# Kernel optimization log

Measured on AMD Instinct MI355X. Metric: run time of the kernel, lower is better.

The kernel has to match this reference:

```python
import jax, jax.numpy as jnp
import numpy as np

H, SK, SV, PK, PV = 12, 16, 16, 4, 8
SCALAR_DIM, PAIR_DIM = 384, 128
SIZES = [SK*H, SK*H, SV*H, PK*H*3, PK*H*3, PV*H*3]  # qkv split sizes
N_LOGITS = 3
SS = (N_LOGITS * SK) ** -0.5                 # scalar logit scale
PS = (N_LOGITS * PK * 4.5) ** -0.5           # point logit scale
PBS = N_LOGITS ** -0.5                       # pair bias scale
EPS = 1e-8


def setup_inputs() -> dict:
    key = jax.random.key(0)
    ks = jax.random.split(key, 16)
    b, n = 1, 768
    scalar_feats = jax.random.normal(ks[0], (b, n, SCALAR_DIM), jnp.float32)
    pair_feats = jax.random.normal(ks[1], (b, n, n, PAIR_DIM), jnp.float32)
    rotations = jax.random.normal(ks[2], (b, n, 3, 3), jnp.float32)
    translations = jax.random.normal(ks[3], (b, n, 3), jnp.float32)
    mask = jnp.ones((b, n), dtype=bool)
    d_qkv = sum(SIZES)
    sc = SCALAR_DIM ** -0.5
    Wqkv = jax.random.normal(ks[4], (SCALAR_DIM, d_qkv), jnp.float32) * sc
    Wpb = jax.random.normal(ks[5], (PAIR_DIM, H), jnp.float32) * PAIR_DIM ** -0.5
    point_weights = jnp.full((1, H, 1, 1), float(np.log(np.e - 1.0)), jnp.float32)
    dim_out = H * (PAIR_DIM + SV + 4 * PV)  # 2112
    Wout = jax.random.normal(ks[6], (dim_out, SCALAR_DIM), jnp.float32) * dim_out ** -0.5
    bout = jnp.zeros((SCALAR_DIM,), jnp.float32)
    Wp1 = jax.random.normal(ks[7], (3 * H, PAIR_DIM), jnp.float32) * (3 * H) ** -0.5
    bp1 = jnp.zeros((PAIR_DIM,), jnp.float32)
    Wp2 = jax.random.normal(ks[8], (PAIR_DIM, PAIR_DIM), jnp.float32) * PAIR_DIM ** -0.5
    bp2 = jnp.zeros((PAIR_DIM,), jnp.float32)
    return dict(scalar_feats=scalar_feats, pair_feats=pair_feats, rotations=rotations,
                translations=translations, mask=mask, Wqkv=Wqkv, Wpb=Wpb,
                point_weights=point_weights, Wout=Wout, bout=bout,
                Wp1=Wp1, bp1=bp1, Wp2=Wp2, bp2=bp2)


def _heads(x, b, n, d):
    # b n (h d) -> b h n d
    return x.reshape(b, n, H, d).transpose(0, 2, 1, 3)


def _merge(x):
    # b h n d -> b n (h d)
    b, h, n, d = x.shape
    return x.transpose(0, 2, 1, 3).reshape(b, n, h * d)


def ipa_forward(scalar_feats, pair_feats, rotations, translations, mask,
                Wqkv, Wpb, point_weights, Wout, bout, Wp1, bp1, Wp2, bp2):
    b, n, _ = scalar_feats.shape
    qkv = scalar_feats @ Wqkv
    offs = np.cumsum([0] + SIZES)
    qs, ks_, vs, qp, kp, vp = [qkv[..., offs[i]:offs[i + 1]] for i in range(6)]
    qs, ks_, vs = _heads(qs, b, n, SK), _heads(ks_, b, n, SK), _heads(vs, b, n, SV)

    def to_global_points(p, d):
        p = p.reshape(b, n, H * d, 3)                       # ... (d c) -> ... d c
        p = jnp.einsum('bixy,bidy->bidx', rotations, p) + translations[:, :, None, :]
        return p.reshape(b, n, H, d, 3).transpose(0, 2, 1, 3, 4)  # b h n d 3

    qp, kp = to_global_points(qp, PK), to_global_points(kp, PK)
    vp = to_global_points(vp, PV)

    scalar_logits = jnp.einsum('bhid,bhjd->bhij', qs, ks_)
    pair_bias = jnp.einsum('bijd,dh->bhij', pair_feats, Wpb)
    point_logits = jnp.einsum('bhidc,bhjdc->bhij', qp, kp) * jax.nn.softplus(point_weights)

    m2 = mask[:, None, :, None] & mask[:, None, None, :]    # b 1 i j
    neg = -jnp.finfo(scalar_logits.dtype).max
    scalar_logits = jnp.where(m2, scalar_logits, neg)
    point_logits = jnp.where(m2, point_logits, neg)
    pair_bias = jnp.where(m2, pair_bias, neg)

    attn = jax.nn.softmax(SS * scalar_logits + PS * point_logits + PBS * pair_bias, axis=-1)

    res_scalar = jnp.einsum('bhij,bhjd->bhid', attn, vs)
    res_pair = jnp.einsum('bhij,bijd->bhid', attn, pair_feats)
    res_pts = jnp.einsum('bhij,bhjdc->bhidc', attn, vp)
    # inverse rigid: R^T (p - t)
    local = jnp.einsum('biyx,bhidy->bhidx', rotations,
                       res_pts - translations[:, None, :, None, :])
    pts_norm = jnp.sqrt(jnp.sum(local ** 2, axis=-1) + EPS)  # safe_norm

    feats = jnp.concatenate([
        _merge(res_scalar),                                   # b n h*SV
        _merge(res_pair),                                     # b n h*PAIR_DIM
        _merge(local.reshape(b, H, n, PV * 3)),               # b n h*PV*3
        _merge(pts_norm),                                     # b n h*PV
    ], axis=-1)
    scalar_out = feats @ Wout + bout

    edge = jnp.concatenate([attn,
                            jax.nn.softmax(point_logits, axis=-1),
                            jax.nn.softmax(scalar_logits, axis=-1)], axis=1)
    edge = edge.transpose(0, 2, 3, 1)                         # b i j (3h)
    pair_out = jax.nn.gelu(edge @ Wp1 + bp1, approximate=False) @ Wp2 + bp2
    return scalar_out, pair_out


def reference(scalar_feats, pair_feats, rotations, translations, mask,
              Wqkv, Wpb, point_weights, Wout, bout, Wp1, bp1, Wp2, bp2):
    return ipa_forward(scalar_feats, pair_feats, rotations, translations, mask,
                       Wqkv, Wpb, point_weights, Wout, bout, Wp1, bp1, Wp2, bp2)
```

## Files before the change

### kernel.cpp

```cpp
#include <hip/hip_runtime.h>
#include <hip/hip_bf16.h>
#include <math.h>

#define NRES 768
#define NH 12
#define DQKV 1152
#define PAIRD 128
#define SCD 384
#define DOUTF 2112

#define SS_C 0.14433756729740643f
#define PS_C 0.13608276348795434f
#define PBS_C 0.5773502691896258f

typedef __attribute__((ext_vector_type(4))) float f32x4;
typedef __attribute__((ext_vector_type(8))) short s16x8;

__device__ __forceinline__ unsigned short f2bf(float x) {
  union { float f; unsigned u; } v; v.f = x;
  unsigned r = (v.u + 0x7fffu + ((v.u >> 16) & 1u)) >> 16;
  return (unsigned short)r;
}

__global__ __launch_bounds__(256) void gemm_f32(
    const float* __restrict__ A, const float* __restrict__ B,
    const float* __restrict__ bias, float* __restrict__ C,
    int M, int Nn, int K)
{
  __shared__ __align__(16) float As[16][68];
  __shared__ __align__(16) float Bs[16][68];
  int t = threadIdx.x;
  int m0 = blockIdx.y * 64, n0 = blockIdx.x * 64;
  int tx = t & 15, ty = t >> 4;
  float acc[4][4] = {};
  int am = t >> 2, ak = (t & 3) * 4;
  int bk = t >> 4, bn = (t & 15) * 4;
  for (int k0 = 0; k0 < K; k0 += 16) {
    float4 a4 = *(const float4*)(A + (size_t)(m0 + am) * K + k0 + ak);
    As[ak + 0][am] = a4.x; As[ak + 1][am] = a4.y;
    As[ak + 2][am] = a4.z; As[ak + 3][am] = a4.w;
    float4 b4 = *(const float4*)(B + (size_t)(k0 + bk) * Nn + n0 + bn);
    *(float4*)&Bs[bk][bn] = b4;
    __syncthreads();
#pragma unroll
    for (int k = 0; k < 16; ++k) {
      float4 av = *(float4*)&As[k][ty * 4];
      float4 bv = *(float4*)&Bs[k][tx * 4];
      float ar[4] = {av.x, av.y, av.z, av.w};
      float br[4] = {bv.x, bv.y, bv.z, bv.w};
#pragma unroll
      for (int r = 0; r < 4; ++r)
#pragma unroll
        for (int c = 0; c < 4; ++c)
          acc[r][c] += ar[r] * br[c];
    }
    __syncthreads();
  }
#pragma unroll
  for (int r = 0; r < 4; ++r) {
    int m = m0 + ty * 4 + r;
#pragma unroll
    for (int c = 0; c < 4; ++c) {
      int n = n0 + tx * 4 + c;
      float v = acc[r][c];
      if (bias) v += bias[n];
      C[(size_t)m * Nn + n] = v;
    }
  }
}

__global__ __launch_bounds__(256) void wt_kernel(
    const float* __restrict__ W, unsigned short* __restrict__ Wt)
{
  __shared__ float tile[32][33];
  int k0 = blockIdx.x * 32, n0 = blockIdx.y * 32;
  int t = threadIdx.x;
  int x = t & 31, y = t >> 5;
#pragma unroll
  for (int r = 0; r < 32; r += 8)
    tile[y + r][x] = W[(size_t)(k0 + y + r) * SCD + n0 + x];
  __syncthreads();
#pragma unroll
  for (int r = 0; r < 32; r += 8)
    Wt[(size_t)(n0 + y + r) * DOUTF + k0 + x] = f2bf(tile[x][y + r]);
}

__global__ __launch_bounds__(192) void points_kernel(
    const float* __restrict__ qkv, const float* __restrict__ rot,
    const float* __restrict__ trans, float* __restrict__ QP,
    float* __restrict__ KP, float* __restrict__ VP)
{
  int i = blockIdx.x;
  int t = threadIdx.x;
  const float* R = rot + (size_t)i * 9;
  const float* T = trans + (size_t)i * 3;
  int base; float* outp;
  if (t < 48) { int h = t >> 2, d = t & 3; base = 576 + (h * 4 + d) * 3;
    outp = QP + ((size_t)h * NRES + i) * 12 + d * 3; }
  else if (t < 96) { int u = t - 48; int h = u >> 2, d = u & 3; base = 720 + (h * 4 + d) * 3;
    outp = KP + ((size_t)h * NRES + i) * 12 + d * 3; }
  else { int u = t - 96; int h = u >> 3, d = u & 7; base = 864 + (h * 8 + d) * 3;
    outp = VP + ((size_t)h * NRES + i) * 24 + d * 3; }
  const float* p = qkv + (size_t)i * DQKV + base;
  float p0 = p[0], p1 = p[1], p2 = p[2];
#pragma unroll
  for (int x = 0; x < 3; ++x)
    outp[x] = R[x * 3 + 0] * p0 + R[x * 3 + 1] * p1 + R[x * 3 + 2] * p2 + T[x];
}

__global__ __launch_bounds__(256) void vt_kernel(
    const float* __restrict__ qkv, const float* __restrict__ VP,
    unsigned short* __restrict__ Vt)
{
  int b = blockIdx.x;
  int h = b / 48, o = b % 48;
  int t = threadIdx.x;
  for (int p = 0; p < 3; ++p) {
    int j = p * 256 + t;
    float v;
    if (o < 16) v = qkv[(size_t)j * DQKV + 384 + h * 16 + o];
    else if (o < 40) v = VP[((size_t)h * NRES + j) * 24 + (o - 16)];
    else v = 0.f;
    Vt[((size_t)h * 48 + o) * NRES + j] = f2bf(v);
  }
}

__global__ __launch_bounds__(256) void pair_bias_kernel(
    const float* __restrict__ pair, const float* __restrict__ Wpb,
    float* __restrict__ Lb)
{
  __shared__ __align__(16) unsigned short Bt[64][136];
  int jt = blockIdx.x, i = blockIdx.y;
  int j0 = jt * 64;
  int t = threadIdx.x;
  int lane = t & 63, w = t >> 6;
  int n15 = lane & 15, q = lane >> 4;
  s16x8 wf[4];
#pragma unroll
  for (int ks = 0; ks < 4; ++ks) {
#pragma unroll
    for (int jj = 0; jj < 8; ++jj) {
      int k = ks * 32 + q * 8 + jj;
      float v = (n15 < 12) ? Wpb[k * 12 + n15] : 0.f;
      wf[ks][jj] = (short)f2bf(v);
    }
  }
  {
    int dq = t & 31, jb = t >> 5;
    for (int p = 0; p < 8; ++p) {
      int j = p * 8 + jb;
      float4 v = *(const float4*)(pair + ((size_t)i * NRES + j0 + j) * PAIRD + dq * 4);
      unsigned lo = (unsigned)f2bf(v.x) | ((unsigned)f2bf(v.y) << 16);
      unsigned hi = (unsigned)f2bf(v.z) | ((unsigned)f2bf(v.w) << 16);
      uint2 pk; pk.x = lo; pk.y = hi;
      *(uint2*)&Bt[j][dq * 4] = pk;
    }
  }
  __syncthreads();
  f32x4 acc = {0.f, 0.f, 0.f, 0.f};
  int m = w * 16 + n15;
#pragma unroll
  for (int ks = 0; ks < 4; ++ks) {
    s16x8 af = *(const s16x8*)&Bt[m][ks * 32 + q * 8];
    acc = __builtin_amdgcn_mfma_f32_16x16x32_bf16(af, wf[ks], acc, 0, 0, 0);
  }
  if (n15 < 12) {
    int j = j0 + w * 16 + q * 4;
    float4 st; st.x = acc[0]; st.y = acc[1]; st.z = acc[2]; st.w = acc[3];
    *(float4*)(Lb + ((size_t)n15 * NRES + i) * NRES + j) = st;
  }
}

__global__ __launch_bounds__(256) void logits_softmax_kernel(
    const float* __restrict__ qkv, const float* __restrict__ QP,
    const float* __restrict__ KP, const float* __restrict__ pw,
    const float* __restrict__ Lb, unsigned short* __restrict__ attn_b,
    unsigned short* __restrict__ sp_b, unsigned short* __restrict__ ss_b)
{
  int i = blockIdx.x, h = blockIdx.y;
  int t = threadIdx.x;
  __shared__ float q_sh[28];
  if (t < 28) {
    if (t < 16) q_sh[t] = qkv[(size_t)i * DQKV + h * 16 + t];
    else q_sh[t] = QP[((size_t)h * NRES + i) * 12 + (t - 16)];
  }
  __syncthreads();
  float spw = log1pf(expf(pw[h]));
  size_t off = ((size_t)h * NRES + i) * NRES;
  float s[3], p[3], c[3];
#pragma unroll
  for (int e = 0; e < 3; ++e) {
    int j = t + e * 256;
    float kr[16];
    const float* kq = qkv + (size_t)j * DQKV + 192 + h * 16;
    *(float4*)&kr[0]  = *(const float4*)(kq + 0);
    *(float4*)&kr[4]  = *(const float4*)(kq + 4);
    *(float4*)&kr[8]  = *(const float4*)(kq + 8);
    *(float4*)&kr[12] = *(const float4*)(kq + 12);
    float sv = 0.f;
#pragma unroll
    for (int d = 0; d < 16; ++d) sv += q_sh[d] * kr[d];
    float kp[12];
    const float* kpp = KP + ((size_t)h * NRES + j) * 12;
    *(float4*)&kp[0] = *(const float4*)(kpp + 0);
    *(float4*)&kp[4] = *(const float4*)(kpp + 4);
    *(float4*)&kp[8] = *(const float4*)(kpp + 8);
    float pv = 0.f;
#pragma unroll
    for (int d = 0; d < 12; ++d) pv += q_sh[16 + d] * kp[d];
    pv *= spw;
    float bv = Lb[off + j];
    s[e] = sv; p[e] = pv;
    c[e] = SS_C * sv + PS_C * pv + PBS_C * bv;
  }
  __shared__ float redmax[4][3];
  __shared__ float redsum[4][3];
  float ms = fmaxf(fmaxf(s[0], s[1]), s[2]);
  float mp = fmaxf(fmaxf(p[0], p[1]), p[2]);
  float mc = fmaxf(fmaxf(c[0], c[1]), c[2]);
#pragma unroll
  for (int o = 32; o > 0; o >>= 1) {
    ms = fmaxf(ms, __shfl_down(ms, o));
    mp = fmaxf(mp, __shfl_down(mp, o));
    mc = fmaxf(mc, __shfl_down(mc, o));
  }
  int wv = t >> 6;
  if ((t & 63) == 0) { redmax[wv][0] = ms; redmax[wv][1] = mp; redmax[wv][2] = mc; }
  __syncthreads();
  ms = fmaxf(fmaxf(redmax[0][0], redmax[1][0]), fmaxf(redmax[2][0], redmax[3][0]));
  mp = fmaxf(fmaxf(redmax[0][1], redmax[1][1]), fmaxf(redmax[2][1], redmax[3][1]));
  mc = fmaxf(fmaxf(redmax[0][2], redmax[1][2]), fmaxf(redmax[2][2], redmax[3][2]));
  float es[3], ep[3], ec[3];
  float sums = 0.f, sump = 0.f, sumc = 0.f;
#pragma unroll
  for (int e = 0; e < 3; ++e) {
    es[e] = expf(s[e] - ms); sums += es[e];
    ep[e] = expf(p[e] - mp); sump += ep[e];
    ec[e] = expf(c[e] - mc); sumc += ec[e];
  }
#pragma unroll
  for (int o = 32; o > 0; o >>= 1) {
    sums += __shfl_down(sums, o);
    sump += __shfl_down(sump, o);
    sumc += __shfl_down(sumc, o);
  }
  if ((t & 63) == 0) { redsum[wv][0] = sums; redsum[wv][1] = sump; redsum[wv][2] = sumc; }
  __syncthreads();
  sums = redsum[0][0] + redsum[1][0] + redsum[2][0] + redsum[3][0];
  sump = redsum[0][1] + redsum[1][1] + redsum[2][1] + redsum[3][1];
  sumc = redsum[0][2] + redsum[1][2] + redsum[2][2] + redsum[3][2];
  float rs = 1.f / sums, rp = 1.f / sump, rc = 1.f / sumc;
#pragma unroll
  for (int e = 0; e < 3; ++e) {
    int j = t + e * 256;
    ss_b[off + j]   = f2bf(es[e] * rs);
    sp_b[off + j]   = f2bf(ep[e] * rp);
    attn_b[off + j] = f2bf(ec[e] * rc);
  }
}

__global__ __launch_bounds__(192) void res_sv_kernel(
    const unsigned short* __restrict__ attn, const unsigned short* __restrict__ Vt,
    float* __restrict__ res_sv)
{
  __shared__ __align__(16) unsigned short A_lds[16][72];
  __shared__ __align__(16) unsigned short B_lds[48][72];
  int it = blockIdx.x, h = blockIdx.y;
  int i0 = it * 16;
  int t = threadIdx.x;
  int lane = t & 63, w = t >> 6;
  int n15 = lane & 15, q = lane >> 4;
  f32x4 acc = {0.f, 0.f, 0.f, 0.f};
  for (int jt = 0; jt < 12; ++jt) {
    int j0 = jt * 64;
    __syncthreads();
    for (int idx = t; idx < 512; idx += 192) {
      int r = idx >> 5, j2 = idx & 31;
      *(unsigned*)&A_lds[r][j2 * 2] =
          *(const unsigned*)&attn[((size_t)h * NRES + i0 + r) * NRES + j0 + j2 * 2];
    }
    for (int idx = t; idx < 1536; idx += 192) {
      int o = idx >> 5, j2 = idx & 31;
      *(unsigned*)&B_lds[o][j2 * 2] =
          *(const unsigned*)&Vt[((size_t)h * 48 + o) * NRES + j0 + j2 * 2];
    }
    __syncthreads();
#pragma unroll
    for (int ks = 0; ks < 2; ++ks) {
      s16x8 af = *(const s16x8*)&A_lds[n15][ks * 32 + q * 8];
      s16x8 bf = *(const s16x8*)&B_lds[w * 16 + n15][ks * 32 + q * 8];
      acc = __builtin_amdgcn_mfma_f32_16x16x32_bf16(af, bf, acc, 0, 0, 0);
    }
  }
  int o = w * 16 + n15;
  if (o < 40) {
#pragma unroll
    for (int r = 0; r < 4; ++r) {
      int i = i0 + q * 4 + r;
      res_sv[((size_t)h * NRES + i) * 40 + o] = acc[r];
    }
  }
}

__global__ __launch_bounds__(256) void res_pair_kernel(
    const unsigned short* __restrict__ attn, const float* __restrict__ pair,
    float* __restrict__ res_pair)
{
  __shared__ __align__(16) unsigned short A_lds[16][72];
  __shared__ __align__(16) unsigned short B_lds[64][132];
  int i = blockIdx.x;
  int t = threadIdx.x;
  int lane = t & 63, w = t >> 6;
  int n15 = lane & 15, q = lane >> 4;
  for (int idx = t; idx < 4 * 72; idx += 256)
    A_lds[12 + idx / 72][idx % 72] = 0;
  f32x4 acc[2];
  acc[0] = (f32x4){0.f, 0.f, 0.f, 0.f};
  acc[1] = (f32x4){0.f, 0.f, 0.f, 0.f};
  for (int jt = 0; jt < 12; ++jt) {
    int j0 = jt * 64;
    __syncthreads();
    for (int idx = t; idx < 384; idx += 256) {
      int r = idx >> 5, j2 = idx & 31;
      *(unsigned*)&A_lds[r][j2 * 2] =
          *(const unsigned*)&attn[((size_t)r * NRES + i) * NRES + j0 + j2 * 2];
    }
    {
      int oq = t & 31, jb = t >> 5;
      for (int p = 0; p < 8; ++p) {
        int j = p * 8 + jb;
        float4 v = *(const float4*)(pair + ((size_t)i * NRES + j0 + j) * PAIRD + oq * 4);
        unsigned lo = (unsigned)f2bf(v.x) | ((unsigned)f2bf(v.y) << 16);
        unsigned hi = (unsigned)f2bf(v.z) | ((unsigned)f2bf(v.w) << 16);
        uint2 pk; pk.x = lo; pk.y = hi;
        *(uint2*)&B_lds[j][oq * 4] = pk;
      }
    }
    __syncthreads();
#pragma unroll
    for (int ks = 0; ks < 2; ++ks) {
      s16x8 af = *(const s16x8*)&A_lds[n15][ks * 32 + q * 8];
#pragma unroll
      for (int nt = 0; nt < 2; ++nt) {
        int o = (w * 2 + nt) * 16 + n15;
        s16x8 bf;
#pragma unroll
        for (int jj = 0; jj < 8; ++jj)
          bf[jj] = (short)B_lds[ks * 32 + q * 8 + jj][o];
        acc[nt] = __builtin_amdgcn_mfma_f32_16x16x32_bf16(af, bf, acc[nt], 0, 0, 0);
      }
    }
  }
#pragma unroll
  for (int nt = 0; nt < 2; ++nt) {
    int o = (w * 2 + nt) * 16 + n15;
#pragma unroll
    for (int r = 0; r < 4; ++r) {
      int hh = q * 4 + r;
      if (hh < 12)
        res_pair[((size_t)hh * NRES + i) * PAIRD + o] = acc[nt][r];
    }
  }
}

__global__ __launch_bounds__(256) void feats_kernel(
    const float* __restrict__ res_sv, const float* __restrict__ res_pair,
    const float* __restrict__ rot, const float* __restrict__ trans,
    unsigned short* __restrict__ feats)
{
  int i = blockIdx.x;
  int t = threadIdx.x;
  unsigned short* F = feats + (size_t)i * DOUTF;
  if (t < 192) {
    int h = t >> 4, d = t & 15;
    F[t] = f2bf(res_sv[((size_t)h * NRES + i) * 40 + d]);
  }
  for (int e = 0; e < 6; ++e) {
    int idx = e * 256 + t;
    int h = idx >> 7, o = idx & 127;
    F[192 + idx] = f2bf(res_pair[((size_t)h * NRES + i) * PAIRD + o]);
  }
  if (t < 96) {
    int h = t >> 3, d = t & 7;
    const float* R = rot + (size_t)i * 9;
    const float* T = trans + (size_t)i * 3;
    const float* pp = res_sv + ((size_t)h * NRES + i) * 40 + 16 + d * 3;
    float p0 = pp[0] - T[0], p1 = pp[1] - T[1], p2 = pp[2] - T[2];
    float l0 = R[0] * p0 + R[3] * p1 + R[6] * p2;
    float l1 = R[1] * p0 + R[4] * p1 + R[7] * p2;
    float l2 = R[2] * p0 + R[5] * p1 + R[8] * p2;
    F[1728 + h * 24 + d * 3 + 0] = f2bf(l0);
    F[1728 + h * 24 + d * 3 + 1] = f2bf(l1);
    F[1728 + h * 24 + d * 3 + 2] = f2bf(l2);
    F[2016 + h * 8 + d] = f2bf(sqrtf(l0 * l0 + l1 * l1 + l2 * l2 + 1e-8f));
  }
}

__global__ __launch_bounds__(256) void gemm_out_mfma(
    const unsigned short* __restrict__ A, const unsigned short* __restrict__ Bt,
    const float* __restrict__ bias, float* __restrict__ C)
{
  __shared__ __align__(16) unsigned short A_lds[64][72];
  __shared__ __align__(16) unsigned short B_lds[64][72];
  int m0 = blockIdx.y * 64, n0 = blockIdx.x * 64;
  int t = threadIdx.x;
  int lane = t & 63, w = t >> 6;
  int n15 = lane & 15, q = lane >> 4;
  f32x4 acc[4];
#pragma unroll
  for (int nt = 0; nt < 4; ++nt) acc[nt] = (f32x4){0.f, 0.f, 0.f, 0.f};
  for (int k0 = 0; k0 < DOUTF; k0 += 64) {
    __syncthreads();
#pragma unroll
    for (int u = 0; u < 2; ++u) {
      int idx = t + u * 256;
      int r = idx >> 3, c = (idx & 7) * 8;
      *(s16x8*)&A_lds[r][c] = *(const s16x8*)&A[(size_t)(m0 + r) * DOUTF + k0 + c];
      *(s16x8*)&B_lds[r][c] = *(const s16x8*)&Bt[(size_t)(n0 + r) * DOUTF + k0 + c];
    }
    __syncthreads();
#pragma unroll
    for (int ks = 0; ks < 2; ++ks) {
      s16x8 af = *(const s16x8*)&A_lds[w * 16 + n15][ks * 32 + q * 8];
#pragma unroll
      for (int nt = 0; nt < 4; ++nt) {
        s16x8 bf = *(const s16x8*)&B_lds[nt * 16 + n15][ks * 32 + q * 8];
        acc[nt] = __builtin_amdgcn_mfma_f32_16x16x32_bf16(af, bf, acc[nt], 0, 0, 0);
      }
    }
  }
#pragma unroll
  for (int nt = 0; nt < 4; ++nt) {
    int n = n0 + nt * 16 + n15;
    float bv = bias[n];
#pragma unroll
    for (int r = 0; r < 4; ++r) {
      int m = m0 + w * 16 + q * 4 + r;
      C[(size_t)m * SCD + n] = acc[nt][r] + bv;
    }
  }
}

__global__ __launch_bounds__(256) void mlp_kernel(
    const unsigned short* __restrict__ attn, const unsigned short* __restrict__ sp,
    const unsigned short* __restrict__ ss, const float* __restrict__ Wp1,
    const float* __restrict__ bp1, const float* __restrict__ Wp2,
    const float* __restrict__ bp2, float* __restrict__ out)
{
  __shared__ __align__(16) unsigned short E_lds[32][72];
  __shared__ __align__(16) unsigned short A_lds[32][136];
  int t = threadIdx.x;
  int lane = t & 63, w = t >> 6;
  int n15 = lane & 15, q = lane >> 4;
  for (int idx = t; idx < 32 * 36; idx += 256) {
    int j = idx / 36, k = 36 + idx % 36;
    E_lds[j][k] = 0;
  }
  s16x8 w1f[2][2], w2f[4][2];
#pragma unroll
  for (int ks = 0; ks < 2; ++ks)
#pragma unroll
    for (int nt = 0; nt < 2; ++nt) {
      int nn = (w * 2 + nt) * 16 + n15;
#pragma unroll
      for (int jj = 0; jj < 8; ++jj) {
        int k = ks * 32 + q * 8 + jj;
        w1f[ks][nt][jj] = (k < 36) ? (short)f2bf(Wp1[(size_t)k * 128 + nn]) : (short)0;
      }
    }
#pragma unroll
  for (int ks = 0; ks < 4; ++ks)
#pragma unroll
    for (int nt = 0; nt < 2; ++nt) {
      int nn = (w * 2 + nt) * 16 + n15;
#pragma unroll
      for (int jj = 0; jj < 8; ++jj) {
        int k = ks * 32 + q * 8 + jj;
        w2f[ks][nt][jj] = (short)f2bf(Wp2[(size_t)k * 128 + nn]);
      }
    }
  float b1v[2], b2v[2];
#pragma unroll
  for (int nt = 0; nt < 2; ++nt) {
    int nn = (w * 2 + nt) * 16 + n15;
    b1v[nt] = bp1[nn];
    b2v[nt] = bp2[nn];
  }
  const unsigned short* bufs[3] = {attn, sp, ss};
  for (int tile = blockIdx.x; tile < NRES * 24; tile += gridDim.x) {
    int i = tile / 24, j0 = (tile % 24) * 32;
    __syncthreads();
    {
      int j = t & 31, c0 = t >> 5;
      for (int p = 0; p < 5; ++p) {
        int c = p * 8 + c0;
        if (c < 36) {
          int hh = c % 12;
          const unsigned short* src = bufs[c / 12];
          E_lds[j][c] = src[((size_t)hh * NRES + i) * NRES + j0 + j];
        }
      }
    }
    __syncthreads();
    f32x4 c1[2][2];
#pragma unroll
    for (int mt = 0; mt < 2; ++mt) {
#pragma unroll
      for (int nt = 0; nt < 2; ++nt) c1[mt][nt] = (f32x4){0.f, 0.f, 0.f, 0.f};
#pragma unroll
      for (int ks = 0; ks < 2; ++ks) {
        s16x8 af = *(const s16x8*)&E_lds[mt * 16 + n15][ks * 32 + q * 8];
#pragma unroll
        for (int nt = 0; nt < 2; ++nt)
          c1[mt][nt] = __builtin_amdgcn_mfma_f32_16x16x32_bf16(af, w1f[ks][nt], c1[mt][nt], 0, 0, 0);
      }
    }
#pragma unroll
    for (int mt = 0; mt < 2; ++mt)
#pragma unroll
      for (int nt = 0; nt < 2; ++nt) {
        int o = (w * 2 + nt) * 16 + n15;
#pragma unroll
        for (int r = 0; r < 4; ++r) {
          float x = c1[mt][nt][r] + b1v[nt];
          float g = 0.5f * x * (1.f + erff(x * 0.70710678118654752f));
          A_lds[mt * 16 + q * 4 + r][o] = f2bf(g);
        }
      }
    __syncthreads();
    f32x4 c2[2][2];
#pragma unroll
    for (int mt = 0; mt < 2; ++mt) {
#pragma unroll
      for (int nt = 0; nt < 2; ++nt) c2[mt][nt] = (f32x4){0.f, 0.f, 0.f, 0.f};
#pragma unroll
      for (int ks = 0; ks < 4; ++ks) {
        s16x8 af = *(const s16x8*)&A_lds[mt * 16 + n15][ks * 32 + q * 8];
#pragma unroll
        for (int nt = 0; nt < 2; ++nt)
          c2[mt][nt] = __builtin_amdgcn_mfma_f32_16x16x32_bf16(af, w2f[ks][nt], c2[mt][nt], 0, 0, 0);
      }
    }
#pragma unroll
    for (int mt = 0; mt < 2; ++mt)
#pragma unroll
      for (int nt = 0; nt < 2; ++nt) {
        int o = (w * 2 + nt) * 16 + n15;
        int jb = j0 + mt * 16 + q * 4;
#pragma unroll
        for (int r = 0; r < 4; ++r)
          out[((size_t)i * NRES + jb + r) * PAIRD + o] = c2[mt][nt][r] + b2v[nt];
      }
  }
}

extern "C" void kernel_launch(void* const* d_in, const int* in_sizes, int n_in,
                              void* d_out, int out_size, void* d_ws, size_t ws_size,
                              hipStream_t stream) {
  const float* scalar_feats = (const float*)d_in[0];
  const float* pair  = (const float*)d_in[1];
  const float* rot   = (const float*)d_in[2];
  const float* trans = (const float*)d_in[3];
  const float* Wqkv  = (const float*)d_in[5];
  const float* Wpb   = (const float*)d_in[6];
  const float* pw    = (const float*)d_in[7];
  const float* Wout  = (const float*)d_in[8];
  const float* bout  = (const float*)d_in[9];
  const float* Wp1   = (const float*)d_in[10];
  const float* bp1   = (const float*)d_in[11];
  const float* Wp2   = (const float*)d_in[12];
  const float* bp2   = (const float*)d_in[13];
  float* out = (float*)d_out;
  float* ws = (float*)d_ws;

  float* qkv = ws;
  float* QP  = ws + 884736;
  float* KP  = ws + 995328;
  float* VP  = ws + 1105920;
  unsigned short* Vt = (unsigned short*)(ws + 1327104);
  float* Lb  = ws + 1548288;
  unsigned short* attn_b = (unsigned short*)(ws + 8626176);
  unsigned short* sp_b   = (unsigned short*)(ws + 12165120);
  unsigned short* ss_b   = (unsigned short*)(ws + 15704064);
  float* res_sv   = ws + 19243008;
  float* res_pair = ws + 19611648;
  unsigned short* feats_b = (unsigned short*)(ws + 20791296);
  unsigned short* Wout_t  = (unsigned short*)(ws + 21602304);

  wt_kernel<<<dim3(DOUTF / 32, SCD / 32), 256, 0, stream>>>(Wout, Wout_t);
  gemm_f32<<<dim3(1152 / 64, 768 / 64), 256, 0, stream>>>(
      scalar_feats, Wqkv, nullptr, qkv, 768, 1152, 384);
  points_kernel<<<768, 192, 0, stream>>>(qkv, rot, trans, QP, KP, VP);
  vt_kernel<<<576, 256, 0, stream>>>(qkv, VP, Vt);
  pair_bias_kernel<<<dim3(12, 768), 256, 0, stream>>>(pair, Wpb, Lb);
  logits_softmax_kernel<<<dim3(768, 12), 256, 0, stream>>>(
      qkv, QP, KP, pw, Lb, attn_b, sp_b, ss_b);
  res_sv_kernel<<<dim3(48, 12), 192, 0, stream>>>(attn_b, Vt, res_sv);
  res_pair_kernel<<<768, 256, 0, stream>>>(attn_b, pair, res_pair);
  feats_kernel<<<768, 256, 0, stream>>>(res_sv, res_pair, rot, trans, feats_b);
  gemm_out_mfma<<<dim3(SCD / 64, 768 / 64), 256, 0, stream>>>(
      feats_b, Wout_t, bout, out);
  mlp_kernel<<<2048, 256, 0, stream>>>(attn_b, sp_b, ss_b, Wp1, bp1, Wp2, bp2, out + 294912);
}
```

Baseline: 922.1 us.

## Use split-bf16 MFMA for QKV GEMM, cache bf16 pair, batch logits rows

After: 916.8 us. About the same (-0.6%).

```diff
diff --git a/kernel.cpp b/kernel.cpp
--- a/kernel.cpp
+++ b/kernel.cpp
@@ -21,51 +21,94 @@
   unsigned r = (v.u + 0x7fffu + ((v.u >> 16) & 1u)) >> 16;
   return (unsigned short)r;
 }
-
-__global__ __launch_bounds__(256) void gemm_f32(
-    const float* __restrict__ A, const float* __restrict__ B,
+__device__ __forceinline__ float bf2f(unsigned short h) {
+  union { unsigned u; float f; } v; v.u = (unsigned)h << 16;
+  return v.f;
+}
+
+__global__ __launch_bounds__(256) void gemm_bf16(
+    const unsigned short* __restrict__ A, const unsigned short* __restrict__ Bt,
     const float* __restrict__ bias, float* __restrict__ C,
     int M, int Nn, int K)
 {
-  __shared__ __align__(16) float As[16][68];
-  __shared__ __align__(16) float Bs[16][68];
-  int t = threadIdx.x;
+  __shared__ __align__(16) unsigned short A_lds[64][72];
+  __shared__ __align__(16) unsigned short B_lds[64][72];
   int m0 = blockIdx.y * 64, n0 = blockIdx.x * 64;
-  int tx = t & 15, ty = t >> 4;
-  float acc[4][4] = {};
-  int am = t >> 2, ak = (t & 3) * 4;
-  int bk = t >> 4, bn = (t & 15) * 4;
-  for (int k0 = 0; k0 < K; k0 += 16) {
-    float4 a4 = *(const float4*)(A + (size_t)(m0 + am) * K + k0 + ak);
-    As[ak + 0][am] = a4.x; As[ak + 1][am] = a4.y;
-    As[ak + 2][am] = a4.z; As[ak + 3][am] = a4.w;
-    float4 b4 = *(const float4*)(B + (size_t)(k0 + bk) * Nn + n0 + bn);
-    *(float4*)&Bs[bk][bn] = b4;
-    __syncthreads();
-#pragma unroll
-    for (int k = 0; k < 16; ++k) {
-      float4 av = *(float4*)&As[k][ty * 4];
-      float4 bv = *(float4*)&Bs[k][tx * 4];
-      float ar[4] = {av.x, av.y, av.z, av.w};
-      float br[4] = {bv.x, bv.y, bv.z, bv.w};
-#pragma unroll
-      for (int r = 0; r < 4; ++r)
-#pragma unroll
-        for (int c = 0; c < 4; ++c)
-          acc[r][c] += ar[r] * br[c];
-    }
-    __syncthreads();
-  }
-#pragma unroll
-  for (int r = 0; r < 4; ++r) {
-    int m = m0 + ty * 4 + r;
-#pragma unroll
-    for (int c = 0; c < 4; ++c) {
-      int n = n0 + tx * 4 + c;
-      float v = acc[r][c];
-      if (bias) v += bias[n];
-      C[(size_t)m * Nn + n] = v;
-    }
+  int t = threadIdx.x;
+  int lane = t & 63, w = t >> 6;
+  int n15 = lane & 15, q = lane >> 4;
+  f32x4 acc[4];
+#pragma unroll
+  for (int nt = 0; nt < 4; ++nt) acc[nt] = (f32x4){0.f, 0.f, 0.f, 0.f};
+  for (int k0 = 0; k0 < K; k0 += 64) {
+    __syncthreads();
+#pragma unroll
+    for (int u = 0; u < 2; ++u) {
+      int idx = t + u * 256;
+      int r = idx >> 3, c = (idx & 7) * 8;
+      *(s16x8*)&A_lds[r][c] = *(const s16x8*)&A[(size_t)(m0 + r) * K + k0 + c];
+      *(s16x8*)&B_lds[r][c] = *(const s16x8*)&Bt[(size_t)(n0 + r) * K + k0 + c];
+    }
+    __syncthreads();
+#pragma unroll
+    for (int ks = 0; ks < 2; ++ks) {
+      s16x8 af = *(const s16x8*)&A_lds[w * 16 + n15][ks * 32 + q * 8];
+#pragma unroll
+      for (int nt = 0; nt < 4; ++nt) {
+        s16x8 bf = *(const s16x8*)&B_lds[nt * 16 + n15][ks * 32 + q * 8];
+        acc[nt] = __builtin_amdgcn_mfma_f32_16x16x32_bf16(af, bf, acc[nt], 0, 0, 0);
+      }
+    }
+  }
+#pragma unroll
+  for (int nt = 0; nt < 4; ++nt) {
+    int n = n0 + nt * 16 + n15;
+    float bv = bias ? bias[n] : 0.f;
+#pragma unroll
+    for (int r = 0; r < 4; ++r) {
+      int m = m0 + w * 16 + q * 4 + r;
+      C[(size_t)m * Nn + n] = acc[nt][r] + bv;
+    }
+  }
+}
+
+__global__ __launch_bounds__(256) void prep_wqkv_kernel(
+    const float* __restrict__ W, unsigned short* __restrict__ Bt)
+{
+  __shared__ float tile[32][33];
+  int k0 = blockIdx.x * 32, n0 = blockIdx.y * 32;
+  int t = threadIdx.x;
+  int x = t & 31, y = t >> 5;
+#pragma unroll
+  for (int r = 0; r < 32; r += 8)
+    tile[y + r][x] = W[(size_t)(k0 + y + r) * DQKV + n0 + x];
+  __syncthreads();
+#pragma unroll
+  for (int r = 0; r < 32; r += 8) {
+    float v = tile[x][y + r];
+    unsigned short hi = f2bf(v);
+    unsigned short lo = f2bf(v - bf2f(hi));
+    size_t nrow = (size_t)(n0 + y + r) * 1152;
+    Bt[nrow + k0 + x]       = hi;
+    Bt[nrow + 384 + k0 + x] = lo;
+    Bt[nrow + 768 + k0 + x] = hi;
+  }
+}
+
+__global__ __launch_bounds__(128) void prep_a_kernel(
+    const float* __restrict__ A, unsigned short* __restrict__ Ap)
+{
+  int i = blockIdx.x, t = threadIdx.x;
+#pragma unroll
+  for (int p = 0; p < 3; ++p) {
+    int c = t + p * 128;
+    float v = A[(size_t)i * SCD + c];
+    unsigned short hi = f2bf(v);
+    unsigned short lo = f2bf(v - bf2f(hi));
+    size_t row = (size_t)i * 1152;
+    Ap[row + c]       = hi;
+    Ap[row + 384 + c] = hi;
+    Ap[row + 768 + c] = lo;
   }
 }
 
@@ -88,7 +131,7 @@
 __global__ __launch_bounds__(192) void points_kernel(
     const float* __restrict__ qkv, const float* __restrict__ rot,
     const float* __restrict__ trans, float* __restrict__ QP,
-    float* __restrict__ KP, float* __restrict__ VP)
+    float* __restrict__ KP, float* __restrict__ VP, float* __restrict__ Kq)
 {
   int i = blockIdx.x;
   int t = threadIdx.x;
@@ -106,6 +149,10 @@
 #pragma unroll
   for (int x = 0; x < 3; ++x)
     outp[x] = R[x * 3 + 0] * p0 + R[x * 3 + 1] * p1 + R[x * 3 + 2] * p2 + T[x];
+  {
+    int h = t >> 4, d = t & 15;
+    Kq[((size_t)h * NRES + i) * 16 + d] = qkv[(size_t)i * DQKV + 192 + h * 16 + d];
+  }
 }
 
 __global__ __launch_bounds__(256) void vt_kernel(
@@ -127,7 +174,7 @@
 
 __global__ __launch_bounds__(256) void pair_bias_kernel(
     const float* __restrict__ pair, const float* __restrict__ Wpb,
-    float* __restrict__ Lb)
+    float* __restrict__ Lb, unsigned short* __restrict__ pair_b)
 {
   __shared__ __align__(16) unsigned short Bt[64][136];
   int jt = blockIdx.x, i = blockIdx.y;
@@ -154,6 +201,7 @@
       unsigned hi = (unsigned)f2bf(v.z) | ((unsigned)f2bf(v.w) << 16);
       uint2 pk; pk.x = lo; pk.y = hi;
       *(uint2*)&Bt[j][dq * 4] = pk;
+      *(uint2*)&pair_b[((size_t)i * NRES + j0 + j) * PAIRD + dq * 4] = pk;
     }
   }
   __syncthreads();
@@ -171,91 +219,109 @@
   }
 }
 
+#define RL 4
 __global__ __launch_bounds__(256) void logits_softmax_kernel(
-    const float* __restrict__ qkv, const float* __restrict__ QP,
-    const float* __restrict__ KP, const float* __restrict__ pw,
-    const float* __restrict__ Lb, unsigned short* __restrict__ attn_b,
-    unsigned short* __restrict__ sp_b, unsigned short* __restrict__ ss_b)
-{
-  int i = blockIdx.x, h = blockIdx.y;
-  int t = threadIdx.x;
-  __shared__ float q_sh[28];
-  if (t < 28) {
-    if (t < 16) q_sh[t] = qkv[(size_t)i * DQKV + h * 16 + t];
-    else q_sh[t] = QP[((size_t)h * NRES + i) * 12 + (t - 16)];
+    const float* __restrict__ qkv, const float* __restrict__ Kq,
+    const float* __restrict__ QP, const float* __restrict__ KP,
+    const float* __restrict__ pw, const float* __restrict__ Lb,
+    unsigned short* __restrict__ attn_b, unsigned short* __restrict__ sp_b,
+    unsigned short* __restrict__ ss_b)
+{
+  int it = blockIdx.x, h = blockIdx.y;
+  int i0 = it * RL;
+  int t = threadIdx.x;
+  __shared__ float q_sh[RL][28];
+  if (t < RL * 28) {
+    int r = t / 28, c = t % 28;
+    q_sh[r][c] = (c < 16) ? qkv[(size_t)(i0 + r) * DQKV + h * 16 + c]
+                          : QP[((size_t)h * NRES + i0 + r) * 12 + (c - 16)];
   }
   __syncthreads();
   float spw = log1pf(expf(pw[h]));
-  size_t off = ((size_t)h * NRES + i) * NRES;
-  float s[3], p[3], c[3];
+  float s[RL][3], p[RL][3], c[RL][3];
 #pragma unroll
   for (int e = 0; e < 3; ++e) {
     int j = t + e * 256;
     float kr[16];
-    const float* kq = qkv + (size_t)j * DQKV + 192 + h * 16;
+    const float* kq = Kq + ((size_t)h * NRES + j) * 16;
     *(float4*)&kr[0]  = *(const float4*)(kq + 0);
     *(float4*)&kr[4]  = *(const float4*)(kq + 4);
     *(float4*)&kr[8]  = *(const float4*)(kq + 8);
     *(float4*)&kr[12] = *(const float4*)(kq + 12);
-    float sv = 0.f;
-#pragma unroll
-    for (int d = 0; d < 16; ++d) sv += q_sh[d] * kr[d];
     float kp[12];
     const float* kpp = KP + ((size_t)h * NRES + j) * 12;
     *(float4*)&kp[0] = *(const float4*)(kpp + 0);
     *(float4*)&kp[4] = *(const float4*)(kpp + 4);
     *(float4*)&kp[8] = *(const float4*)(kpp + 8);
-    float pv = 0.f;
-#pragma unroll
-    for (int d = 0; d < 12; ++d) pv += q_sh[16 + d] * kp[d];
-    pv *= spw;
-    float bv = Lb[off + j];
-    s[e] = sv; p[e] = pv;
-    c[e] = SS_C * sv + PS_C * pv + PBS_C * bv;
-  }
-  __shared__ float redmax[4][3];
-  __shared__ float redsum[4][3];
-  float ms = fmaxf(fmaxf(s[0], s[1]), s[2]);
-  float mp = fmaxf(fmaxf(p[0], p[1]), p[2]);
-  float mc = fmaxf(fmaxf(c[0], c[1]), c[2]);
-#pragma unroll
-  for (int o = 32; o > 0; o >>= 1) {
-    ms = fmaxf(ms, __shfl_down(ms, o));
-    mp = fmaxf(mp, __shfl_down(mp, o));
-    mc = fmaxf(mc, __shfl_down(mc, o));
-  }
+#pragma unroll
+    for (int r = 0; r < RL; ++r) {
+      float sv = 0.f;
+#pragma unroll
+      for (int d = 0; d < 16; ++d) sv += q_sh[r][d] * kr[d];
+      float pv = 0.f;
+#pragma unroll
+      for (int d = 0; d < 12; ++d) pv += q_sh[r][16 + d] * kp[d];
+      pv *= spw;
+      float bv = Lb[((size_t)h * NRES + i0 + r) * NRES + j];
+      s[r][e] = sv; p[r][e] = pv;
+      c[r][e] = SS_C * sv + PS_C * pv + PBS_C * bv;
+    }
+  }
+  __shared__ float redm[4][RL][3];
+  __shared__ float redsu[4][RL][3];
   int wv = t >> 6;
-  if ((t & 63) == 0) { redmax[wv][0] = ms; redmax[wv][1] = mp; redmax[wv][2] = mc; }
+#pragma unroll
+  for (int r = 0; r < RL; ++r) {
+    float ms = fmaxf(fmaxf(s[r][0], s[r][1]), s[r][2]);
+    float mp = fmaxf(fmaxf(p[r][0], p[r][1]), p[r][2]);
+    float mc = fmaxf(fmaxf(c[r][0], c[r][1]), c[r][2]);
+#pragma unroll
+    for (int o = 32; o > 0; o >>= 1) {
+      ms = fmaxf(ms, __shfl_down(ms, o));
+      mp = fmaxf(mp, __shfl_down(mp, o));
+      mc = fmaxf(mc, __shfl_down(mc, o));
+    }
+    if ((t & 63) == 0) { redm[wv][r][0] = ms; redm[wv][r][1] = mp; redm[wv][r][2] = mc; }
+  }
   __syncthreads();
-  ms = fmaxf(fmaxf(redmax[0][0], redmax[1][0]), fmaxf(redmax[2][0], redmax[3][0]));
-  mp = fmaxf(fmaxf(redmax[0][1], redmax[1][1]), fmaxf(redmax[2][1], redmax[3][1]));
-  mc = fmaxf(fmaxf(redmax[0][2], redmax[1][2]), fmaxf(redmax[2][2], redmax[3][2]));
-  float es[3], ep[3], ec[3];
-  float sums = 0.f, sump = 0.f, sumc = 0.f;
-#pragma unroll
-  for (int e = 0; e < 3; ++e) {
-    es[e] = expf(s[e] - ms); sums += es[e];
-    ep[e] = expf(p[e] - mp); sump += ep[e];
-    ec[e] = expf(c[e] - mc); sumc += ec[e];
-  }
-#pragma unroll
-  for (int o = 32; o > 0; o >>= 1) {
-    sums += __shfl_down(sums, o);
-    sump += __shfl_down(sump, o);
-    sumc += __shfl_down(sumc, o);
-  }
-  if ((t & 63) == 0) { redsum[wv][0] = sums; redsum[wv][1] = sump; redsum[wv][2] = sumc; }
+  float Ms[RL], Mp[RL], Mc[RL];
+#pragma unroll
+  for (int r = 0; r < RL; ++r) {
+    Ms[r] = fmaxf(fmaxf(redm[0][r][0], redm[1][r][0]), fmaxf(redm[2][r][0], redm[3][r][0]));
+    Mp[r] = fmaxf(fmaxf(redm[0][r][1], redm[1][r][1]), fmaxf(redm[2][r][1], redm[3][r][1]));
+    Mc[r] = fmaxf(fmaxf(redm[0][r][2], redm[1][r][2]), fmaxf(redm[2][r][2], redm[3][r][2]));
+  }
+#pragma unroll
+  for (int r = 0; r < RL; ++r) {
+    float sums = 0.f, sump = 0.f, sumc = 0.f;
+#pragma unroll
+    for (int e = 0; e < 3; ++e) {
+      float es = expf(s[r][e] - Ms[r]); s[r][e] = es; sums += es;
+      float ep = expf(p[r][e] - Mp[r]); p[r][e] = ep; sump += ep;
+      float ec = expf(c[r][e] - Mc[r]); c[r][e] = ec; sumc += ec;
+    }
+#pragma unroll
+    for (int o = 32; o > 0; o >>= 1) {
+      sums += __shfl_down(sums, o);
+      sump += __shfl_down(sump, o);
+      sumc += __shfl_down(sumc, o);
+    }
+    if ((t & 63) == 0) { redsu[wv][r][0] = sums; redsu[wv][r][1] = sump; redsu[wv][r][2] = sumc; }
+  }
   __syncthreads();
-  sums = redsum[0][0] + redsum[1][0] + redsum[2][0] + redsum[3][0];
-  sump = redsum[0][1] + redsum[1][1] + redsum[2][1] + redsum[3][1];
-  sumc = redsum[0][2] + redsum[1][2] + redsum[2][2] + redsum[3][2];
-  float rs = 1.f / sums, rp = 1.f / sump, rc = 1.f / sumc;
-#pragma unroll
-  for (int e = 0; e < 3; ++e) {
-    int j = t + e * 256;
-    ss_b[off + j]   = f2bf(es[e] * rs);
-    sp_b[off + j]   = f2bf(ep[e] * rp);
-    attn_b[off + j] = f2bf(ec[e] * rc);
+#pragma unroll
+  for (int r = 0; r < RL; ++r) {
+    float rs = 1.f / (redsu[0][r][0] + redsu[1][r][0] + redsu[2][r][0] + redsu[3][r][0]);
+    float rp = 1.f / (redsu[0][r][1] + redsu[1][r][1] + redsu[2][r][1] + redsu[3][r][1]);
+    float rc = 1.f / (redsu[0][r][2] + redsu[1][r][2] + redsu[2][r][2] + redsu[3][r][2]);
+    size_t off = ((size_t)h * NRES + i0 + r) * NRES;
+#pragma unroll
+    for (int e = 0; e < 3; ++e) {
+      int j = t + e * 256;
+      ss_b[off + j]   = f2bf(s[r][e] * rs);
+      sp_b[off + j]   = f2bf(p[r][e] * rp);
+      attn_b[off + j] = f2bf(c[r][e] * rc);
+    }
   }
 }
 
@@ -303,7 +369,7 @@
 }
 
 __global__ __launch_bounds__(256) void res_pair_kernel(
-    const unsigned short* __restrict__ attn, const float* __restrict__ pair,
+    const unsigned short* __restrict__ attn, const unsigned short* __restrict__ pair_b,
     float* __restrict__ res_pair)
 {
   __shared__ __align__(16) unsigned short A_lds[16][72];
@@ -326,14 +392,12 @@
           *(const unsigned*)&attn[((size_t)r * NRES + i) * NRES + j0 + j2 * 2];
     }
     {
-      int oq = t & 31, jb = t >> 5;
-      for (int p = 0; p < 8; ++p) {
-        int j = p * 8 + jb;
-        float4 v = *(const float4*)(pair + ((size_t)i * NRES + j0 + j) * PAIRD + oq * 4);
-        unsigned lo = (unsigned)f2bf(v.x) | ((unsigned)f2bf(v.y) << 16);
-        unsigned hi = (unsigned)f2bf(v.z) | ((unsigned)f2bf(v.w) << 16);
-        uint2 pk; pk.x = lo; pk.y = hi;
-        *(uint2*)&B_lds[j][oq * 4] = pk;
+      int o8 = t & 15, jb = t >> 4;
+#pragma unroll
+      for (int p = 0; p < 4; ++p) {
+        int j = p * 16 + jb;
+        *(s16x8*)&B_lds[j][o8 * 8] =
+            *(const s16x8*)&pair_b[((size_t)i * NRES + j0 + j) * PAIRD + o8 * 8];
       }
     }
     __syncthreads();
@@ -396,64 +460,19 @@
   }
 }
 
-__global__ __launch_bounds__(256) void gemm_out_mfma(
-    const unsigned short* __restrict__ A, const unsigned short* __restrict__ Bt,
-    const float* __restrict__ bias, float* __restrict__ C)
-{
-  __shared__ __align__(16) unsigned short A_lds[64][72];
-  __shared__ __align__(16) unsigned short B_lds[64][72];
-  int m0 = blockIdx.y * 64, n0 = blockIdx.x * 64;
-  int t = threadIdx.x;
-  int lane = t & 63, w = t >> 6;
-  int n15 = lane & 15, q = lane >> 4;
-  f32x4 acc[4];
-#pragma unroll
-  for (int nt = 0; nt < 4; ++nt) acc[nt] = (f32x4){0.f, 0.f, 0.f, 0.f};
-  for (int k0 = 0; k0 < DOUTF; k0 += 64) {
-    __syncthreads();
-#pragma unroll
-    for (int u = 0; u < 2; ++u) {
-      int idx = t + u * 256;
-      int r = idx >> 3, c = (idx & 7) * 8;
-      *(s16x8*)&A_lds[r][c] = *(const s16x8*)&A[(size_t)(m0 + r) * DOUTF + k0 + c];
-      *(s16x8*)&B_lds[r][c] = *(const s16x8*)&Bt[(size_t)(n0 + r) * DOUTF + k0 + c];
-    }
-    __syncthreads();
-#pragma unroll
-    for (int ks = 0; ks < 2; ++ks) {
-      s16x8 af = *(const s16x8*)&A_lds[w * 16 + n15][ks * 32 + q * 8];
-#pragma unroll
-      for (int nt = 0; nt < 4; ++nt) {
-        s16x8 bf = *(const s16x8*)&B_lds[nt * 16 + n15][ks * 32 + q * 8];
-        acc[nt] = __builtin_amdgcn_mfma_f32_16x16x32_bf16(af, bf, acc[nt], 0, 0, 0);
-      }
-    }
-  }
-#pragma unroll
-  for (int nt = 0; nt < 4; ++nt) {
-    int n = n0 + nt * 16 + n15;
-    float bv = bias[n];
-#pragma unroll
-    for (int r = 0; r < 4; ++r) {
-      int m = m0 + w * 16 + q * 4 + r;
-      C[(size_t)m * SCD + n] = acc[nt][r] + bv;
-    }
-  }
-}
-
 __global__ __launch_bounds__(256) void mlp_kernel(
     const unsigned short* __restrict__ attn, const unsigned short* __restrict__ sp,
     const unsigned short* __restrict__ ss, const float* __restrict__ Wp1,
     const float* __restrict__ bp1, const float* __restrict__ Wp2,
     const float* __restrict__ bp2, float* __restrict__ out)
 {
-  __shared__ __align__(16) unsigned short E_lds[32][72];
-  __shared__ __align__(16) unsigned short A_lds[32][136];
+  __shared__ __align__(16) unsigned short E_lds[64][72];
+  __shared__ __align__(16) unsigned short A_lds[64][136];
   int t = threadIdx.x;
   int lane = t & 63, w = t >> 6;
   int n15 = lane & 15, q = lane >> 4;
-  for (int idx = t; idx < 32 * 36; idx += 256) {
-    int j = idx / 36, k = 36 + idx % 36;
+  for (int idx = t; idx < 64 * 28; idx += 256) {
+    int j = idx / 28, k = 36 + idx % 28;
     E_lds[j][k] = 0;
   }
   s16x8 w1f[2][2], w2f[4][2];
@@ -487,24 +506,23 @@
     b2v[nt] = bp2[nn];
   }
   const unsigned short* bufs[3] = {attn, sp, ss};
-  for (int tile = blockIdx.x; tile < NRES * 24; tile += gridDim.x) {
-    int i = tile / 24, j0 = (tile % 24) * 32;
+  for (int tile = blockIdx.x; tile < NRES * 12; tile += gridDim.x) {
+    int i = tile / 12, j0 = (tile % 12) * 64;
     __syncthreads();
     {
-      int j = t & 31, c0 = t >> 5;
-      for (int p = 0; p < 5; ++p) {
-        int c = p * 8 + c0;
-        if (c < 36) {
-          int hh = c % 12;
-          const unsigned short* src = bufs[c / 12];
-          E_lds[j][c] = src[((size_t)hh * NRES + i) * NRES + j0 + j];
-        }
-      }
-    }
-    __syncthreads();
-    f32x4 c1[2][2];
-#pragma unroll
-    for (int mt = 0; mt < 2; ++mt) {
+      int j = t & 63, cb = t >> 6;
+#pragma unroll
+      for (int p = 0; p < 9; ++p) {
+        int cc = cb * 9 + p;
+        int hh = cc % 12;
+        const unsigned short* src = bufs[cc / 12];
+        E_lds[j][cc] = src[((size_t)hh * NRES + i) * NRES + j0 + j];
+      }
+    }
+    __syncthreads();
+    f32x4 c1[4][2];
+#pragma unroll
+    for (int mt = 0; mt < 4; ++mt) {
 #pragma unroll
       for (int nt = 0; nt < 2; ++nt) c1[mt][nt] = (f32x4){0.f, 0.f, 0.f, 0.f};
 #pragma unroll
@@ -516,7 +534,7 @@
       }
     }
 #pragma unroll
-    for (int mt = 0; mt < 2; ++mt)
+    for (int mt = 0; mt < 4; ++mt)
 #pragma unroll
       for (int nt = 0; nt < 2; ++nt) {
         int o = (w * 2 + nt) * 16 + n15;
@@ -528,9 +546,9 @@
         }
       }
     __syncthreads();
-    f32x4 c2[2][2];
-#pragma unroll
-    for (int mt = 0; mt < 2; ++mt) {
+    f32x4 c2[4][2];
+#pragma unroll
+    for (int mt = 0; mt < 4; ++mt) {
 #pragma unroll
       for (int nt = 0; nt < 2; ++nt) c2[mt][nt] = (f32x4){0.f, 0.f, 0.f, 0.f};
 #pragma unroll
@@ -542,7 +560,7 @@
       }
     }
 #pragma unroll
-    for (int mt = 0; mt < 2; ++mt)
+    for (int mt = 0; mt < 4; ++mt)
 #pragma unroll
       for (int nt = 0; nt < 2; ++nt) {
         int o = (w * 2 + nt) * 16 + n15;
@@ -586,19 +604,25 @@
   float* res_pair = ws + 19611648;
   unsigned short* feats_b = (unsigned short*)(ws + 20791296);
   unsigned short* Wout_t  = (unsigned short*)(ws + 21602304);
-
+  float* Kq = ws + 22007808;
+  unsigned short* Aprime  = (unsigned short*)(ws + 22155264);
+  unsigned short* Wqkv_t  = (unsigned short*)(ws + 22597632);
+  unsigned short* pair_b  = (unsigned short*)(ws + 23261184);
+
+  prep_wqkv_kernel<<<dim3(SCD / 32, DQKV / 32), 256, 0, stream>>>(Wqkv, Wqkv_t);
+  prep_a_kernel<<<NRES, 128, 0, stream>>>(scalar_feats, Aprime);
+  gemm_bf16<<<dim3(DQKV / 64, NRES / 64), 256, 0, stream>>>(
+      Aprime, Wqkv_t, nullptr, qkv, NRES, DQKV, 1152);
+  points_kernel<<<NRES, 192, 0, stream>>>(qkv, rot, trans, QP, KP, VP, Kq);
+  vt_kernel<<<576, 256, 0, stream>>>(qkv, VP, Vt);
+  pair_bias_kernel<<<dim3(12, NRES), 256, 0, stream>>>(pair, Wpb, Lb, pair_b);
+  logits_softmax_kernel<<<dim3(NRES / RL, 12), 256, 0, stream>>>(
+      qkv, Kq, QP, KP, pw, Lb, attn_b, sp_b, ss_b);
+  res_sv_kernel<<<dim3(48, 12), 192, 0, stream>>>(attn_b, Vt, res_sv);
+  res_pair_kernel<<<NRES, 256, 0, stream>>>(attn_b, pair_b, res_pair);
+  feats_kernel<<<NRES, 256, 0, stream>>>(res_sv, res_pair, rot, trans, feats_b);
   wt_kernel<<<dim3(DOUTF / 32, SCD / 32), 256, 0, stream>>>(Wout, Wout_t);
-  gemm_f32<<<dim3(1152 / 64, 768 / 64), 256, 0, stream>>>(
-      scalar_feats, Wqkv, nullptr, qkv, 768, 1152, 384);
-  points_kernel<<<768, 192, 0, stream>>>(qkv, rot, trans, QP, KP, VP);
-  vt_kernel<<<576, 256, 0, stream>>>(qkv, VP, Vt);
-  pair_bias_kernel<<<dim3(12, 768), 256, 0, stream>>>(pair, Wpb, Lb);
-  logits_softmax_kernel<<<dim3(768, 12), 256, 0, stream>>>(
-      qkv, QP, KP, pw, Lb, attn_b, sp_b, ss_b);
-  res_sv_kernel<<<dim3(48, 12), 192, 0, stream>>>(attn_b, Vt, res_sv);
-  res_pair_kernel<<<768, 256, 0, stream>>>(attn_b, pair, res_pair);
-  feats_kernel<<<768, 256, 0, stream>>>(res_sv, res_pair, rot, trans, feats_b);
-  gemm_out_mfma<<<dim3(SCD / 64, 768 / 64), 256, 0, stream>>>(
-      feats_b, Wout_t, bout, out);
+  gemm_bf16<<<dim3(SCD / 64, NRES / 64), 256, 0, stream>>>(
+      feats_b, Wout_t, bout, out, NRES, SCD, DOUTF);
   mlp_kernel<<<2048, 256, 0, stream>>>(attn_b, sp_b, ss_b, Wp1, bp1, Wp2, bp2, out + 294912);
 }
```
